# Optimization experiments

Hardware: AMD Instinct MI355X
Metric: run time of the kernel (lower is better)

## Reference

```python
import jax, jax.numpy as jnp
import numpy as np

N_NODES = 30000
N_REL = 8
N_EDGES = 131072
IN_FEAT = 512
OUT_FEAT = 512


def setup_inputs() -> dict:
    key = jax.random.key(0)
    k1, k2, k3, k4, k5 = jax.random.split(key, 5)
    x = jax.random.normal(k1, (N_NODES, IN_FEAT), dtype=jnp.float32)
    # per-relation weights [R, in, out] (xavier-ish scale)
    weight = jax.random.normal(k2, (N_REL, IN_FEAT, OUT_FEAT), dtype=jnp.float32) * (2.0 / (IN_FEAT + OUT_FEAT)) ** 0.5
    loop_weight = jax.random.normal(k3, (IN_FEAT, OUT_FEAT), dtype=jnp.float32) * (2.0 / (IN_FEAT + OUT_FEAT)) ** 0.5
    h_bias = jnp.zeros((OUT_FEAT,), dtype=jnp.float32)
    src = jax.random.randint(k4, (N_REL, N_EDGES), 0, N_NODES, dtype=jnp.int32)
    dst = jax.random.randint(k5, (N_REL, N_EDGES), 0, N_NODES, dtype=jnp.int32)
    return {"x": x, "weight": weight, "loop_weight": loop_weight,
            "h_bias": h_bias, "src": src, "dst": dst}


def reference(x, weight, loop_weight, h_bias, src, dst):
    # Per-relation GraphConv(norm='right', weight=W_r):
    #   transform all node feats, gather on src, scatter-sum on dst,
    #   normalize by in-degree (clamped to 1). Relations summed (HeteroGraphConv 'sum').
    xw = jnp.einsum('ni,rio->rno', x, weight)  # [R, N, out]

    def per_rel(xw_r, src_r, dst_r):
        msgs = xw_r[src_r]  # [E, out] gathered messages
        agg = jax.ops.segment_sum(msgs, dst_r, num_segments=N_NODES)
        deg = jax.ops.segment_sum(jnp.ones_like(dst_r, dtype=xw_r.dtype), dst_r,
                                  num_segments=N_NODES)
        return agg / jnp.clip(deg, 1.0)[:, None]

    h = jax.vmap(per_rel)(xw, src, dst).sum(axis=0)  # [N, out]
    h = h + x @ loop_weight + h_bias  # self-loop + bias
    return jax.nn.relu(h)  # activation; dropout=0.0 -> identity
```

## Files before the change

kernel.cpp:

```cpp
#include <hip/hip_runtime.h>
#include <hip/hip_bf16.h>

#define N_NODES 30000
#define N_REL   8
#define N_EDGES 131072
#define FEAT    512
#define KTOT    4608
#define CAP     32

typedef __attribute__((ext_vector_type(8))) __bf16 v8bf;
typedef __attribute__((ext_vector_type(4))) __bf16 v4bf;
typedef __attribute__((ext_vector_type(4))) float  v4f;
typedef __attribute__((ext_vector_type(2))) float  f2;
typedef __attribute__((ext_vector_type(8))) unsigned short u16x8;

static __device__ __forceinline__ void load_lds16(const void* g, void* l) {
  __builtin_amdgcn_global_load_lds(
      (const __attribute__((address_space(1))) void*)g,
      (__attribute__((address_space(3))) void*)l, 16, 0, 0);
}

#define CONV_BLOCKS 15000
#define TR_BLOCKS   2304
#define CNT_BLOCKS  512
__global__ __launch_bounds__(256)
void k_prep(const float* __restrict__ x, const float* __restrict__ w,
            const float* __restrict__ lw, const int* __restrict__ src,
            const int* __restrict__ dst, __bf16* __restrict__ xbf,
            __bf16* __restrict__ Wt, int* __restrict__ cnt,
            unsigned short* __restrict__ slots) {
  __shared__ float t[32][33];
  const int b = blockIdx.x, tid = threadIdx.x;
  if (b < CONV_BLOCKS) {
    int i = b * 256 + tid;
    float4 v = ((const float4*)x)[i];
    v4bf o;
    o[0] = (__bf16)v.x; o[1] = (__bf16)v.y; o[2] = (__bf16)v.z; o[3] = (__bf16)v.w;
    ((v4bf*)xbf)[i] = o;
  } else if (b < CONV_BLOCKS + TR_BLOCKS) {
    int tb = b - CONV_BLOCKS;
    int k0 = (tb % 144) * 32, n0 = (tb / 144) * 32;
    int tx = tid & 31, ty = tid >> 5;
    #pragma unroll
    for (int q = 0; q < 4; ++q) {
      int k = k0 + ty + q * 8, n = n0 + tx;
      float v = (k < 4096) ? w[(size_t)k * 512 + n] : lw[(size_t)(k - 4096) * 512 + n];
      t[ty + q * 8][tx] = v;
    }
    __syncthreads();
    #pragma unroll
    for (int q = 0; q < 4; ++q) {
      int n = n0 + ty + q * 8, k = k0 + tx;
      Wt[(size_t)n * KTOT + k] = (__bf16)t[tx][ty + q * 8];
    }
  } else {
    int cb  = b - CONV_BLOCKS - TR_BLOCKS;
    int rel = cb & 7;
    int q   = cb >> 3;
    int e0  = rel * N_EDGES + (q * 256 + tid) * 8;
    int4 sa = *(const int4*)(src + e0), sb = *(const int4*)(src + e0 + 4);
    int4 da = *(const int4*)(dst + e0), db = *(const int4*)(dst + e0 + 4);
    int ss[8] = {sa.x, sa.y, sa.z, sa.w, sb.x, sb.y, sb.z, sb.w};
    int dd[8] = {da.x, da.y, da.z, da.w, db.x, db.y, db.z, db.w};
    int bb[8], pp[8];
    #pragma unroll
    for (int j = 0; j < 8; ++j) {
      bb[j] = rel * N_NODES + dd[j];
      pp[j] = atomicAdd(&cnt[bb[j]], 1);
    }
    #pragma unroll
    for (int j = 0; j < 8; ++j)
      if (pp[j] < CAP) slots[(size_t)bb[j] * CAP + pp[j]] = (unsigned short)ss[j];
  }
}

__global__ __launch_bounds__(256)
void k_agg_slice(const __bf16* __restrict__ xbf, const int* __restrict__ cnt,
                 const unsigned short* __restrict__ slots,
                 __bf16* __restrict__ out, int nBuckets, int bps) {
  const int bid   = blockIdx.x;
  const int slice = bid / bps;
  const int ib    = bid - slice * bps;
  const int tid   = threadIdx.x;
  const int wave  = tid >> 6, lane = tid & 63;
  const int grp   = lane >> 3;
  const int li    = lane & 7;
  const int w     = ib * 32 + wave * 8 + grp;
  const bool valid = (w < nBuckets);

  int c = 0;
  u16x8 qs[4];
  if (valid) {
    c = cnt[w];
    const unsigned short* sl = slots + (size_t)w * CAP;
    qs[0] = *(const u16x8*)(sl);
    qs[1] = *(const u16x8*)(sl + 8);
    qs[2] = *(const u16x8*)(sl + 16);
    qs[3] = *(const u16x8*)(sl + 24);
  }
  int cc = c < CAP ? c : CAP;
  int cmax = cc;
  cmax = max(cmax, __shfl_xor(cmax, 8));
  cmax = max(cmax, __shfl_xor(cmax, 16));
  cmax = max(cmax, __shfl_xor(cmax, 32));

  const __bf16* xb = xbf + slice * 64 + (size_t)li * 8;
  f2 acc2[4];
  #pragma unroll
  for (int p = 0; p < 4; ++p) acc2[p] = (f2){0.f, 0.f};
  #pragma unroll
  for (int g = 0; g < 4; ++g) {
    if (cmax > g * 8) {
      v8bf r[8];
      #pragma unroll
      for (int j = 0; j < 8; ++j)
        if (cc > g * 8 + j)
          r[j] = *(const v8bf*)(xb + (size_t)qs[g][j] * FEAT);
      #pragma unroll
      for (int j = 0; j < 8; ++j)
        if (cc > g * 8 + j) {
          const unsigned* ru = (const unsigned*)&r[j];
          #pragma unroll
          for (int p = 0; p < 4; ++p) {
            f2 v;
            v[0] = __uint_as_float(ru[p] << 16);
            v[1] = __uint_as_float(ru[p] & 0xffff0000u);
            acc2[p] += v;
          }
        }
    }
  }
  if (valid) {
    float scale = 1.0f / (float)(c > 1 ? c : 1);
    v8bf o;
    #pragma unroll
    for (int p = 0; p < 4; ++p) {
      o[2 * p]     = (__bf16)(acc2[p][0] * scale);
      o[2 * p + 1] = (__bf16)(acc2[p][1] * scale);
    }
    *(v8bf*)(out + (size_t)w * FEAT + slice * 64 + (size_t)li * 8) = o;
  }
}

__global__ __launch_bounds__(256)
void k_aggregate(const __bf16* __restrict__ xbf, const int* __restrict__ cnt,
                 const unsigned short* __restrict__ slots,
                 __bf16* __restrict__ out, int nBuckets) {
  int w = (blockIdx.x * blockDim.x + threadIdx.x) >> 6;
  int lane = threadIdx.x & 63;
  if (w >= nBuckets) return;
  const unsigned short* sl = slots + (size_t)w * CAP;
  u16x8 qs[4];
  qs[0] = *(const u16x8*)(sl);
  qs[1] = *(const u16x8*)(sl + 8);
  qs[2] = *(const u16x8*)(sl + 16);
  qs[3] = *(const u16x8*)(sl + 24);
  int c = cnt[w];
  int cc = c < CAP ? c : CAP;
  const __bf16* xb = xbf + (size_t)lane * 8;
  f2 acc2[4];
  #pragma unroll
  for (int p = 0; p < 4; ++p) acc2[p] = (f2){0.f, 0.f};
  #pragma unroll
  for (int g = 0; g < 4; ++g) {
    if (cc > g * 8) {
      int m = cc - g * 8;
      v8bf r[8];
      #pragma unroll
      for (int j = 0; j < 8; ++j)
        if (m > j) r[j] = *(const v8bf*)(xb + (size_t)qs[g][j] * FEAT);
      #pragma unroll
      for (int j = 0; j < 8; ++j)
        if (m > j) {
          const unsigned* ru = (const unsigned*)&r[j];
          #pragma unroll
          for (int p = 0; p < 4; ++p) {
            f2 v;
            v[0] = __uint_as_float(ru[p] << 16);
            v[1] = __uint_as_float(ru[p] & 0xffff0000u);
            acc2[p] += v;
          }
        }
    }
  }
  float scale = 1.0f / (float)(c > 1 ? c : 1);
  v8bf o;
  #pragma unroll
  for (int p = 0; p < 4; ++p) {
    o[2 * p]     = (__bf16)(acc2[p][0] * scale);
    o[2 * p + 1] = (__bf16)(acc2[p][1] * scale);
  }
  *(v8bf*)(out + (size_t)w * FEAT + lane * 8) = o;
}

template <bool ACCUM, bool FINAL>
__global__ __launch_bounds__(512, 2)
void k_gemm3(const __bf16* __restrict__ A, size_t slabStride,
             const __bf16* __restrict__ Wt, int kTiles,
             const float* __restrict__ bias, float* __restrict__ C) {
  __shared__ __align__(16) char smem[131072];

  const int tid  = threadIdx.x;
  const int wave = tid >> 6, lane = tid & 63;
  const int lr = lane >> 3, lc = lane & 7;
  const int gcs = (lc ^ lr) * 8;
  const int quad = lane >> 4, l15 = lane & 15;
  const int wR2 = wave >> 2;
  const int wC4 = wave & 3;

  const int nwg = gridDim.x;
  const int qq = nwg >> 3, rr = nwg & 7;
  const int xcd = blockIdx.x & 7, oidx = blockIdx.x >> 3;
  const int wg = (xcd < rr ? xcd * (qq + 1) : rr * (qq + 1) + (xcd - rr) * qq) + oidx;
  const int mtile = wg >> 1, ntile = wg & 1;
  const int mBase = mtile * 256, nBase = ntile * 256;

  v4f acc[2][2][4][2];
  #pragma unroll
  for (int a = 0; a < 2; ++a)
    #pragma unroll
    for (int bq = 0; bq < 2; ++bq)
      #pragma unroll
      for (int mi = 0; mi < 4; ++mi)
        #pragma unroll
        for (int ni = 0; ni < 2; ++ni)
          acc[a][bq][mi][ni] = (v4f){0.f, 0.f, 0.f, 0.f};

  auto stageA = [&](int t, int h) {
    __bf16* dst = (__bf16*)(smem + (t & 1) * 65536);
    const int kk = t * 64;
    const __bf16* base = A + (size_t)(kk >> 9) * slabStride + (kk & 511);
    #pragma unroll
    for (int r2 = 0; r2 < 2; ++r2) {
      int rt = h * 128 + r2 * 64 + wave * 8;
      int row = mBase + rt + lr;
      if (row > N_NODES - 1) row = N_NODES - 1;
      load_lds16(base + (size_t)row * FEAT + gcs, dst + rt * 64);
    }
  };
  auto stageB = [&](int t, int h) {
    __bf16* dst = (__bf16*)(smem + (t & 1) * 65536 + 32768);
    const int kk = t * 64;
    #pragma unroll
    for (int r2 = 0; r2 < 2; ++r2) {
      int rt = h * 128 + r2 * 64 + wave * 8;
      int n = nBase + rt + lr;
      load_lds16(Wt + (size_t)n * KTOT + kk + gcs, dst + rt * 64);
    }
  };

  stageA(0, 0); stageB(0, 0); stageB(0, 1); stageA(0, 1);
  asm volatile("s_waitcnt vmcnt(4)" ::: "memory");
  __builtin_amdgcn_s_barrier();
  __builtin_amdgcn_sched_barrier(0);

  for (int t = 0; t < kTiles; ++t) {
    const __bf16* sA = (const __bf16*)(smem + (t & 1) * 65536);
    const __bf16* sB = sA + 16384;
    const bool pf = (t + 1) < kTiles;
    v8bf af[4][2], bf0[2][2], bf1[2][2];

    #pragma unroll
    for (int mi = 0; mi < 4; ++mi)
      #pragma unroll
      for (int ks = 0; ks < 2; ++ks) {
        int m = wR2 * 64 + mi * 16 + l15;
        int q = ks * 4 + quad;
        af[mi][ks] = *(const v8bf*)(sA + m * 64 + ((q ^ (m & 7)) * 8));
      }
    #pragma unroll
    for (int ni = 0; ni < 2; ++ni)
      #pragma unroll
      for (int ks = 0; ks < 2; ++ks) {
        int n = wC4 * 32 + ni * 16 + l15;
        int q = ks * 4 + quad;
        bf0[ni][ks] = *(const v8bf*)(sB + n * 64 + ((q ^ (n & 7)) * 8));
      }
    if (pf) stageA(t + 1, 0);
    __builtin_amdgcn_s_barrier();
    asm volatile("s_waitcnt lgkmcnt(0)" ::: "memory");
    __builtin_amdgcn_sched_barrier(0);
    __builtin_amdgcn_s_setprio(1);
    #pragma unroll
    for (int ks = 0; ks < 2; ++ks)
      #pragma unroll
      for (int mi = 0; mi < 4; ++mi)
        #pragma unroll
        for (int ni = 0; ni < 2; ++ni)
          acc[0][0][mi][ni] = __builtin_amdgcn_mfma_f32_16x16x32_bf16(
              af[mi][ks], bf0[ni][ks], acc[0][0][mi][ni], 0, 0, 0);
    __builtin_amdgcn_s_setprio(0);
    if (pf) asm volatile("s_waitcnt vmcnt(4)" ::: "memory");
    else    asm volatile("s_waitcnt vmcnt(2)" ::: "memory");
    __builtin_amdgcn_s_barrier();
    __builtin_amdgcn_sched_barrier(0);

    #pragma unroll
    for (int ni = 0; ni < 2; ++ni)
      #pragma unroll
      for (int ks = 0; ks < 2; ++ks) {
        int n = 128 + wC4 * 32 + ni * 16 + l15;
        int q = ks * 4 + quad;
        bf1[ni][ks] = *(const v8bf*)(sB + n * 64 + ((q ^ (n & 7)) * 8));
      }
    if (pf) stageB(t + 1, 0);
    __builtin_amdgcn_s_barrier();
    asm volatile("s_waitcnt lgkmcnt(0)" ::: "memory");
    __builtin_amdgcn_sched_barrier(0);
    __builtin_amdgcn_s_setprio(1);
    #pragma unroll
    for (int ks = 0; ks < 2; ++ks)
      #pragma unroll
      for (int mi = 0; mi < 4; ++mi)
        #pragma unroll
        for (int ni = 0; ni < 2; ++ni)
          acc[0][1][mi][ni] = __builtin_amdgcn_mfma_f32_16x16x32_bf16(
              af[mi][ks], bf1[ni][ks], acc[0][1][mi][ni], 0, 0, 0);
    __builtin_amdgcn_s_setprio(0);
    if (pf) asm volatile("s_waitcnt vmcnt(4)" ::: "memory");
    else    asm volatile("s_waitcnt vmcnt(0)" ::: "memory");
    __builtin_amdgcn_s_barrier();
    __builtin_amdgcn_sched_barrier(0);

    #pragma unroll
    for (int mi = 0; mi < 4; ++mi)
      #pragma unroll
      for (int ks = 0; ks < 2; ++ks) {
        int m = 128 + wR2 * 64 + mi * 16 + l15;
        int q = ks * 4 + quad;
        af[mi][ks] = *(const v8bf*)(sA + m * 64 + ((q ^ (m & 7)) * 8));
      }
    if (pf) stageB(t + 1, 1);
    __builtin_amdgcn_s_barrier();
    asm volatile("s_waitcnt lgkmcnt(0)" ::: "memory");
    __builtin_amdgcn_sched_barrier(0);
    __builtin_amdgcn_s_setprio(1);
    #pragma unroll
    for (int ks = 0; ks < 2; ++ks)
      #pragma unroll
      for (int mi = 0; mi < 4; ++mi)
        #pragma unroll
        for (int ni = 0; ni < 2; ++ni)
          acc[1][1][mi][ni] = __builtin_amdgcn_mfma_f32_16x16x32_bf16(
              af[mi][ks], bf1[ni][ks], acc[1][1][mi][ni], 0, 0, 0);
    __builtin_amdgcn_s_setprio(0);
    __builtin_amdgcn_s_barrier();
    __builtin_amdgcn_sched_barrier(0);

    if (pf) stageA(t + 1, 1);
    __builtin_amdgcn_s_barrier();
    __builtin_amdgcn_s_setprio(1);
    #pragma unroll
    for (int ks = 0; ks < 2; ++ks)
      #pragma unroll
      for (int mi = 0; mi < 4; ++mi)
        #pragma unroll
        for (int ni = 0; ni < 2; ++ni)
          acc[1][0][mi][ni] = __builtin_amdgcn_mfma_f32_16x16x32_bf16(
              af[mi][ks], bf0[ni][ks], acc[1][0][mi][ni], 0, 0, 0);
    __builtin_amdgcn_s_setprio(0);
    if (pf) asm volatile("s_waitcnt vmcnt(4)" ::: "memory");
    __builtin_amdgcn_s_barrier();
    __builtin_amdgcn_sched_barrier(0);
  }

  asm volatile("s_waitcnt vmcnt(0)" ::: "memory");
  float* cbuf = (float*)smem;
  const int f4 = tid & 63;
  const int colg = nBase + f4 * 4;
  v4f bias4 = (v4f){0.f, 0.f, 0.f, 0.f};
  if (FINAL) bias4 = *(const v4f*)(bias + colg);
  #pragma unroll
  for (int h = 0; h < 4; ++h) {
    __syncthreads();
    if (wR2 == (h & 1)) {
      const int R = h >> 1;
      #pragma unroll
      for (int Cq = 0; Cq < 2; ++Cq)
        #pragma unroll
        for (int mi = 0; mi < 4; ++mi)
          #pragma unroll
          for (int ni = 0; ni < 2; ++ni)
            #pragma unroll
            for (int e = 0; e < 4; ++e)
              cbuf[(mi * 16 + quad * 4 + e) * 260 + Cq * 128 + wC4 * 32 + ni * 16 + l15] =
                  acc[R][Cq][mi][ni][e];
    }
    __syncthreads();
    #pragma unroll
    for (int i = 0; i < 8; ++i) {
      int rl  = i * 8 + (tid >> 6);
      int row = mBase + h * 64 + rl;
      if (row < N_NODES) {
        v4f v = *(const v4f*)(cbuf + rl * 260 + f4 * 4);
        size_t idx = (size_t)row * FEAT + colg;
        if (ACCUM) v += *(const v4f*)(C + idx);
        if (FINAL) {
          #pragma unroll
          for (int e = 0; e < 4; ++e) v[e] = fmaxf(v[e] + bias4[e], 0.f);
        }
        *(v4f*)(C + idx) = v;
      }
    }
  }
}

template <bool ACCUM, bool FINAL>
__global__ __launch_bounds__(256, 4)
void k_gemm(const __bf16* __restrict__ A, size_t slabStride,
            const __bf16* __restrict__ Wt, int wtStride, int kTiles,
            const float* __restrict__ bias, float* __restrict__ C,
            int mtBase, int mtEnd) {
  __shared__ __align__(16) char smem[33792];
  __bf16* As = (__bf16*)smem;
  __bf16* Bs = (__bf16*)(smem + 16384);

  const int tid  = threadIdx.x;
  const int wave = tid >> 6;
  const int lane = tid & 63;
  const int lr = lane >> 3, lc = lane & 7;
  const int gcs = (lc ^ lr) * 8;
  const int quad = lane >> 4, l15 = lane & 15;
  const int wRow = wave >> 1, wCol = wave & 1;

  const int panel = blockIdx.x >> 5;
  const int w32   = blockIdx.x & 31;
  const int mtile = mtBase + panel * 8 + (w32 & 7);
  const int ntile = w32 >> 3;
  if (mtile >= mtEnd) return;
  const int mBase = mtile * 128;
  const int nBase = ntile * 128;

  v4f acc[4][4];
  #pragma unroll
  for (int i = 0; i < 4; ++i)
    #pragma unroll
    for (int j = 0; j < 4; ++j) acc[i][j] = (v4f){0.f, 0.f, 0.f, 0.f};

  for (int kt = 0; kt < kTiles; ++kt) {
    const int kk = kt * 64;
    const __bf16* aT = A + (size_t)(kk >> 9) * slabStride + (kk & 511);
    #pragma unroll
    for (int t = 0; t < 4; ++t) {
      int chunk = wave * 4 + t;
      int row = mBase + chunk * 8 + lr;
      if (row > N_NODES - 1) row = N_NODES - 1;
      load_lds16(aT + (size_t)row * FEAT + gcs, As + chunk * 512);
      int n = nBase + chunk * 8 + lr;
      load_lds16(Wt + (size_t)n * wtStride + kk + gcs, Bs + chunk * 512);
    }
    __syncthreads();
    #pragma unroll
    for (int ks = 0; ks < 2; ++ks) {
      const int q = ks * 4 + quad;
      v8bf af[4], bfr[4];
      #pragma unroll
      for (int mi = 0; mi < 4; ++mi) {
        int m = wRow * 64 + mi * 16 + l15;
        af[mi] = *(const v8bf*)(As + m * 64 + ((q ^ (m & 7)) * 8));
      }
      #pragma unroll
      for (int ni = 0; ni < 4; ++ni) {
        int n = wCol * 64 + ni * 16 + l15;
        bfr[ni] = *(const v8bf*)(Bs + n * 64 + ((q ^ (n & 7)) * 8));
      }
      #pragma unroll
      for (int mi = 0; mi < 4; ++mi)
        #pragma unroll
        for (int ni = 0; ni < 4; ++ni)
          acc[mi][ni] = __builtin_amdgcn_mfma_f32_16x16x32_bf16(af[mi], bfr[ni], acc[mi][ni], 0, 0, 0);
    }
    __syncthreads();
  }

  float* cbuf = (float*)smem;
  const int f4c  = tid & 31;
  const int colg = nBase + f4c * 4;
  v4f bias4 = (v4f){0.f, 0.f, 0.f, 0.f};
  if (FINAL) bias4 = *(const v4f*)(bias + colg);
  #pragma unroll
  for (int h = 0; h < 2; ++h) {
    if (wRow == h) {
      #pragma unroll
      for (int mi = 0; mi < 4; ++mi) {
        int r0 = mi * 16 + quad * 4;
        #pragma unroll
        for (int ni = 0; ni < 4; ++ni) {
          int c = wCol * 64 + ni * 16 + l15;
          #pragma unroll
          for (int e = 0; e < 4; ++e)
            cbuf[(r0 + e) * 132 + c] = acc[mi][ni][e];
        }
      }
    }
    __syncthreads();
    #pragma unroll
    for (int i = 0; i < 8; ++i) {
      int rh  = (tid >> 5) + 8 * i;
      int row = mBase + h * 64 + rh;
      if (row < N_NODES) {
        v4f v = *(const v4f*)(cbuf + rh * 132 + f4c * 4);
        size_t idx = (size_t)row * FEAT + colg;
        if (ACCUM) v += *(const v4f*)(C + idx);
        if (FINAL) {
          #pragma unroll
          for (int e = 0; e < 4; ++e) v[e] = fmaxf(v[e] + bias4[e], 0.f);
        }
        *(v4f*)(C + idx) = v;
      }
    }
    __syncthreads();
  }
}

extern "C" void kernel_launch(void* const* d_in, const int* in_sizes, int n_in,
                              void* d_out, int out_size, void* d_ws, size_t ws_size,
                              hipStream_t stream) {
  const float* x    = (const float*)d_in[0];
  const float* w    = (const float*)d_in[1];
  const float* lw   = (const float*)d_in[2];
  const float* bias = (const float*)d_in[3];
  const int*   src  = (const int*)d_in[4];
  const int*   dst  = (const int*)d_in[5];
  float* out = (float*)d_out;

  char* ws = (char*)d_ws;
  const size_t SLAB  = (size_t)N_NODES * FEAT;
  const size_t slabB = SLAB * 2;
  const size_t wtB   = (size_t)FEAT * KTOT * 2;
  const size_t cntB  = (size_t)N_REL * N_NODES * 4;
  const size_t slotB = (size_t)N_REL * N_NODES * CAP * 2;
  const size_t fixedB = wtB + cntB + slotB;

  __bf16*         Wt     = (__bf16*)ws;
  int*            cnt    = (int*)(ws + wtB);
  unsigned short* slots  = (unsigned short*)(ws + wtB + cntB);
  __bf16*         slabs  = (__bf16*)(ws + fixedB);

  int nSlab = (int)((ws_size - fixedB) / slabB);
  int g = nSlab - 1;
  if (g > 7) g = 7;
  if (g < 1) g = 1;
  __bf16* xbf = slabs + (size_t)g * SLAB;

  hipMemsetAsync(cnt, 0, cntB, stream);
  k_prep<<<CONV_BLOCKS + TR_BLOCKS + CNT_BLOCKS, 256, 0, stream>>>(
      x, w, lw, src, dst, xbf, Wt, cnt, slots);

  if (g == 7) {
    const int mt256 = (N_NODES + 255) / 256;
    const int grid3 = mt256 * 2;
    const int bps1 = (7 * N_NODES + 31) / 32;
    k_agg_slice<<<8 * bps1, 256, 0, stream>>>(xbf, cnt, slots,
                                              slabs, 7 * N_NODES, bps1);
    k_gemm3<false, false><<<grid3, 512, 0, stream>>>(
        slabs, SLAB, Wt, 3584 / 64, bias, out);
    const int bps2 = (N_NODES + 31) / 32;
    k_agg_slice<<<8 * bps2, 256, 0, stream>>>(
        xbf, cnt + 7 * N_NODES, slots + (size_t)7 * N_NODES * CAP,
        slabs + (size_t)6 * SLAB, N_NODES, bps2);
    k_gemm3<true, true><<<grid3, 512, 0, stream>>>(
        slabs + (size_t)6 * SLAB, SLAB, Wt + 3584, 1024 / 64, bias, out);
  } else {
    const int nMtiles = (N_NODES + 127) / 128;
    const int gemmGrid = ((nMtiles + 7) / 8) * 32;
    for (int r0 = 0; r0 < N_REL; r0 += g) {
      int gc2 = (N_REL - r0) < g ? (N_REL - r0) : g;
      k_aggregate<<<(gc2 * N_NODES) / 4, 256, 0, stream>>>(
          xbf, cnt + r0 * N_NODES, slots + (size_t)r0 * N_NODES * CAP,
          slabs, gc2 * N_NODES);
      if (r0 == 0)
        k_gemm<false, false><<<gemmGrid, 256, 0, stream>>>(
            slabs, SLAB, Wt + r0 * 512, KTOT, gc2 * 8, bias, out, 0, nMtiles);
      else
        k_gemm<true, false><<<gemmGrid, 256, 0, stream>>>(
            slabs, SLAB, Wt + r0 * 512, KTOT, gc2 * 8, bias, out, 0, nMtiles);
    }
    k_gemm<true, true><<<gemmGrid, 256, 0, stream>>>(xbf, SLAB, Wt + 4096, KTOT,
                                                     8, bias, out, 0, nMtiles);
  }
}
```

Measured before the change: 499.1 us.

## Triple-buffer A tiles in GEMM to prefetch two k-steps ahead

Grows the LDS buffer so the GEMM keeps three A-tile slots and two B-tile slots. A is now prefetched two k-tiles ahead and B one ahead, and the vmcnt waits and prologue are rearranged to match. The goal is to hide more global-load latency behind the MFMA phases. The block now asks for 160 KB of LDS, which likely allows only one block per CU instead of the two requested by the launch bounds, so latency hiding from occupancy is lost.

Result: no change. 498.2 us (-0.2%).

```diff
diff --git a/kernel.cpp b/kernel.cpp
--- a/kernel.cpp
+++ b/kernel.cpp
@@ -193,12 +193,16 @@
   *(v8bf*)(out + (size_t)w * FEAT + lane * 8) = o;
 }
 
+#define A_SLOT_E 16384
+#define B_BASE_E 49152
+
 template <bool ACCUM, bool FINAL>
 __global__ __launch_bounds__(512, 2)
 void k_gemm3(const __bf16* __restrict__ A, size_t slabStride,
              const __bf16* __restrict__ Wt, int kTiles,
              const float* __restrict__ bias, float* __restrict__ C) {
-  __shared__ __align__(16) char smem[131072];
+  __shared__ __align__(16) char smem[163840];
+  __bf16* lds = (__bf16*)smem;
 
   const int tid  = threadIdx.x;
   const int wave = tid >> 6, lane = tid & 63;
@@ -227,7 +231,7 @@
           acc[a][bq][mi][ni] = (v4f){0.f, 0.f, 0.f, 0.f};
 
   auto stageA = [&](int t, int h) {
-    __bf16* dst = (__bf16*)(smem + (t & 1) * 65536);
+    __bf16* dst = lds + (t % 3) * A_SLOT_E;
     const int kk = t * 64;
     const __bf16* base = A + (size_t)(kk >> 9) * slabStride + (kk & 511);
     #pragma unroll
@@ -239,7 +243,7 @@
     }
   };
   auto stageB = [&](int t, int h) {
-    __bf16* dst = (__bf16*)(smem + (t & 1) * 65536 + 32768);
+    __bf16* dst = lds + B_BASE_E + (t & 1) * A_SLOT_E;
     const int kk = t * 64;
     #pragma unroll
     for (int r2 = 0; r2 < 2; ++r2) {
@@ -249,15 +253,22 @@
     }
   };
 
-  stageA(0, 0); stageB(0, 0); stageB(0, 1); stageA(0, 1);
-  asm volatile("s_waitcnt vmcnt(4)" ::: "memory");
+  stageA(0, 0); stageA(0, 1);
+  stageB(0, 0); stageB(0, 1);
+  if (kTiles > 1) {
+    stageA(1, 0); stageA(1, 1);
+    asm volatile("s_waitcnt vmcnt(4)" ::: "memory");
+  } else {
+    asm volatile("s_waitcnt vmcnt(0)" ::: "memory");
+  }
   __builtin_amdgcn_s_barrier();
   __builtin_amdgcn_sched_barrier(0);
 
   for (int t = 0; t < kTiles; ++t) {
-    const __bf16* sA = (const __bf16*)(smem + (t & 1) * 65536);
-    const __bf16* sB = sA + 16384;
-    const bool pf = (t + 1) < kTiles;
+    const __bf16* sA = lds + (t % 3) * A_SLOT_E;
+    const __bf16* sB = lds + B_BASE_E + (t & 1) * A_SLOT_E;
+    const bool pfB = (t + 1) < kTiles;
+    const bool pfA = (t + 2) < kTiles;
     v8bf af[4][2], bf0[2][2], bf1[2][2];
 
     #pragma unroll
@@ -276,7 +287,7 @@
         int q = ks * 4 + quad;
         bf0[ni][ks] = *(const v8bf*)(sB + n * 64 + ((q ^ (n & 7)) * 8));
       }
-    if (pf) stageA(t + 1, 0);
+    if (pfB) stageB(t + 1, 0);
     __builtin_amdgcn_s_barrier();
     asm volatile("s_waitcnt lgkmcnt(0)" ::: "memory");
     __builtin_amdgcn_sched_barrier(0);
@@ -290,8 +301,8 @@
           acc[0][0][mi][ni] = __builtin_amdgcn_mfma_f32_16x16x32_bf16(
               af[mi][ks], bf0[ni][ks], acc[0][0][mi][ni], 0, 0, 0);
     __builtin_amdgcn_s_setprio(0);
-    if (pf) asm volatile("s_waitcnt vmcnt(4)" ::: "memory");
-    else    asm volatile("s_waitcnt vmcnt(2)" ::: "memory");
+    if (pfB) asm volatile("s_waitcnt vmcnt(6)" ::: "memory");
+    else     asm volatile("s_waitcnt vmcnt(0)" ::: "memory");
     __builtin_amdgcn_s_barrier();
     __builtin_amdgcn_sched_barrier(0);
 
@@ -303,7 +314,7 @@
         int q = ks * 4 + quad;
         bf1[ni][ks] = *(const v8bf*)(sB + n * 64 + ((q ^ (n & 7)) * 8));
       }
-    if (pf) stageB(t + 1, 0);
+    if (pfB) stageB(t + 1, 1);
     __builtin_amdgcn_s_barrier();
     asm volatile("s_waitcnt lgkmcnt(0)" ::: "memory");
     __builtin_amdgcn_sched_barrier(0);
@@ -317,8 +328,6 @@
           acc[0][1][mi][ni] = __builtin_amdgcn_mfma_f32_16x16x32_bf16(
               af[mi][ks], bf1[ni][ks], acc[0][1][mi][ni], 0, 0, 0);
     __builtin_amdgcn_s_setprio(0);
-    if (pf) asm volatile("s_waitcnt vmcnt(4)" ::: "memory");
-    else    asm volatile("s_waitcnt vmcnt(0)" ::: "memory");
     __builtin_amdgcn_s_barrier();
     __builtin_amdgcn_sched_barrier(0);
 
@@ -330,7 +339,7 @@
         int q = ks * 4 + quad;
         af[mi][ks] = *(const v8bf*)(sA + m * 64 + ((q ^ (m & 7)) * 8));
       }
-    if (pf) stageB(t + 1, 1);
+    if (pfA) stageA(t + 2, 0);
     __builtin_amdgcn_s_barrier();
     asm volatile("s_waitcnt lgkmcnt(0)" ::: "memory");
     __builtin_amdgcn_sched_barrier(0);
@@ -347,7 +356,7 @@
     __builtin_amdgcn_s_barrier();
     __builtin_amdgcn_sched_barrier(0);
 
-    if (pf) stageA(t + 1, 1);
+    if (pfA) stageA(t + 2, 1);
     __builtin_amdgcn_s_barrier();
     __builtin_amdgcn_s_setprio(1);
     #pragma unroll
@@ -359,7 +368,8 @@
           acc[1][0][mi][ni] = __builtin_amdgcn_mfma_f32_16x16x32_bf16(
               af[mi][ks], bf0[ni][ks], acc[1][0][mi][ni], 0, 0, 0);
     __builtin_amdgcn_s_setprio(0);
-    if (pf) asm volatile("s_waitcnt vmcnt(4)" ::: "memory");
+    if (pfA)      asm volatile("s_waitcnt vmcnt(6)" ::: "memory");
+    else if (pfB) asm volatile("s_waitcnt vmcnt(2)" ::: "memory");
     __builtin_amdgcn_s_barrier();
     __builtin_amdgcn_sched_barrier(0);
   }
```
